# Performance work log

Measured on AMD Instinct MI355X. Metric: run time of the kernel, lower is better.

The kernel has to match this reference:

```python
import jax, jax.numpy as jnp
import numpy as np
from jax import lax


def _conv2d(x, w, b, pad):
    out = lax.conv_general_dilated(x, w, window_strides=(1, 1),
                                   padding=[(pad, pad), (pad, pad)])
    return out + b[None, :, None, None]


def _modulated_deform_conv(x, off_w, off_b, w, b, k, pad):
    """Modulated deformable conv (deformable_groups=1, stride=1, 'same' pad)."""
    B, C, H, W = x.shape
    K2 = k * k
    # offset/mask conv: 3*K2 channels -> (dy, dx, mask_logits)
    om = _conv2d(x, off_w, off_b, pad)              # [B, 3*K2, H, W]
    dy, dx, mlog = om[:, :K2], om[:, K2:2 * K2], om[:, 2 * K2:]
    mask = jax.nn.sigmoid(mlog)                     # [B, K2, H, W]

    xp = jnp.pad(x, ((0, 0), (0, 0), (pad, pad), (pad, pad)))
    Hp, Wp = H + 2 * pad, W + 2 * pad
    Ho, Wo = H, W                                   # stride 1, pad = k//2

    ky, kx = jnp.meshgrid(jnp.arange(k), jnp.arange(k), indexing='ij')
    ky = ky.reshape(1, K2, 1, 1).astype(x.dtype)
    kx = kx.reshape(1, K2, 1, 1).astype(x.dtype)
    iy = jnp.arange(Ho, dtype=x.dtype).reshape(1, 1, Ho, 1)
    ix = jnp.arange(Wo, dtype=x.dtype).reshape(1, 1, 1, Wo)

    py = iy + ky + dy                               # [B, K2, Ho, Wo] sample y (padded coords)
    px = ix + kx + dx                               # [B, K2, Ho, Wo] sample x

    y0f = jnp.floor(py); x0f = jnp.floor(px)
    ty = py - y0f; tx = px - x0f
    y0 = y0f.astype(jnp.int32); x0 = x0f.astype(jnp.int32)
    y1 = y0 + 1; x1 = x0 + 1

    xp_flat = xp.reshape(B, C, Hp * Wp)

    def gather(yi, xi):
        valid = ((yi >= 0) & (yi < Hp) & (xi >= 0) & (xi < Wp)).astype(x.dtype)
        yc = jnp.clip(yi, 0, Hp - 1)
        xc = jnp.clip(xi, 0, Wp - 1)
        idx = (yc * Wp + xc).reshape(B, 1, K2 * Ho * Wo)
        v = jnp.take_along_axis(xp_flat, idx, axis=2).reshape(B, C, K2, Ho, Wo)
        return v * valid[:, None]                   # zero-pad outside

    w00 = ((1 - ty) * (1 - tx))[:, None]
    w01 = ((1 - ty) * tx)[:, None]
    w10 = (ty * (1 - tx))[:, None]
    w11 = (ty * tx)[:, None]

    cols = (gather(y0, x0) * w00 + gather(y0, x1) * w01 +
            gather(y1, x0) * w10 + gather(y1, x1) * w11)
    cols = cols * mask[:, None]                     # [B, C, K2, Ho, Wo]

    O = w.shape[0]
    out = jnp.einsum('bckhw,ock->bohw', cols, w.reshape(O, C, K2))
    return out + b[None, :, None, None]


def setup_inputs() -> dict:
    key = jax.random.key(0)
    ks = jax.random.split(key, 12)
    B, Cin, H, W = 8, 64, 56, 56
    Ch = 128  # out_channels // 2

    def rn(k, shape, scale):
        return jax.random.normal(k, shape, dtype=jnp.float32) * scale

    return {
        'x': rn(ks[0], (B, Cin, H, W), 1.0),
        'w3': rn(ks[1], (Ch, Cin, 3, 3), 0.05),
        'b3': rn(ks[2], (Ch,), 0.05),
        'off3_w': rn(ks[3], (3 * 9, Cin, 3, 3), 0.01),
        'off3_b': rn(ks[4], (3 * 9,), 0.01),
        'w5': rn(ks[5], (Ch, Cin, 5, 5), 0.03),
        'b5': rn(ks[6], (Ch,), 0.05),
        'off5_w': rn(ks[7], (3 * 25, Cin, 5, 5), 0.01),
        'off5_b': rn(ks[8], (3 * 25,), 0.01),
        'sub_w': rn(ks[9], (Ch, Cin, 1, 1), 0.1),
        'sub_b': rn(ks[10], (Ch,), 0.05),
    }


def reference(x, w3, b3, off3_w, off3_b, w5, b5, off5_w, off5_b, sub_w, sub_b):
    x3 = _modulated_deform_conv(x, off3_w, off3_b, w3, b3, k=3, pad=1)
    x5 = _modulated_deform_conv(x, off5_w, off5_b, w5, b5, k=5, pad=2)
    xs = _conv2d(x, sub_w, sub_b, pad=0)            # 1x1 shortcut projection
    x3 = x3 + xs
    x5 = x5 + xs
    out = jnp.concatenate((x3, x5), axis=1)
    return jax.nn.relu(out)
```

## Files before the change

kernel.cpp:

```cpp
#include <hip/hip_runtime.h>
#include <hip/hip_bf16.h>
#include <math.h>

typedef __attribute__((ext_vector_type(8))) short short8;
typedef __attribute__((ext_vector_type(4))) float f32x4;

#define US_XP    0
#define N_XP     (8*60*60*64)
#define US_WOFF  (US_XP + N_XP)
#define N_WOFF   (26*2*8*64*8)
#define US_W5    (US_WOFF + N_WOFF)
#define N_W5     (26*2*8*64*8)
#define US_W3    (US_W5 + N_W5)
#define N_W3     (10*2*8*64*8)
#define US_TOT   (US_W3 + N_W3)
#define FB_BYTES (((US_TOT*2) + 15) & ~15)
#define F_BOM    0
#define F_B5     128
#define F_B3     256
#define N_ITEMS  (8*34*3136)
#define F_OFFS   384
#define F_WTS    (F_OFFS + N_ITEMS*4)

__device__ __forceinline__ unsigned short f2bf(float f) {
    union { float f; unsigned u; } v; v.f = f;
    unsigned r = v.u + 0x7FFFu + ((v.u >> 16) & 1u);
    return (unsigned short)(r >> 16);
}
__device__ __forceinline__ unsigned pack2(float lo, float hi) {
    __hip_bfloat162 h = __float22bfloat162_rn(make_float2(lo, hi));
    return *(unsigned*)&h;
}
__device__ __forceinline__ unsigned blend2(unsigned a, unsigned b, unsigned c, unsigned d,
                                           float w00, float w01, float w10, float w11) {
    float lo = __uint_as_float(a << 16) * w00 + __uint_as_float(b << 16) * w01
             + __uint_as_float(c << 16) * w10 + __uint_as_float(d << 16) * w11;
    float hi = __uint_as_float(a & 0xffff0000u) * w00 + __uint_as_float(b & 0xffff0000u) * w01
             + __uint_as_float(c & 0xffff0000u) * w10 + __uint_as_float(d & 0xffff0000u) * w11;
    return pack2(lo, hi);
}

__global__ __launch_bounds__(256) void xpose(const float* __restrict__ x,
                                             unsigned short* __restrict__ xp)
{
    __shared__ float ld[64*65];
    const int b   = blockIdx.y;
    const int px0 = blockIdx.x * 64;
    const int t   = threadIdx.x;
#pragma unroll
    for (int c0 = 0; c0 < 64; c0 += 4) {
        const int c = c0 + (t >> 6);
        const int p = t & 63;
        ld[c*65 + p] = x[((size_t)(b*64 + c))*3136 + px0 + p];
    }
    __syncthreads();
    const int lp = t >> 2;
    const int ch0 = (t & 3) * 16;
    const int px = px0 + lp;
    const int oy = px/56, ox = px - oy*56;
    unsigned short* dst = xp + ((size_t)b*3600 + (oy+2)*60 + (ox+2))*64 + ch0;
    unsigned short tmp[16];
#pragma unroll
    for (int k = 0; k < 16; ++k) tmp[k] = f2bf(ld[(ch0 + k)*65 + lp]);
    *(uint4*)dst       = *(uint4*)&tmp[0];
    *(uint4*)(dst + 8) = *(uint4*)&tmp[8];
}

__global__ __launch_bounds__(256) void prep_w(
    const float* __restrict__ w3, const float* __restrict__ b3,
    const float* __restrict__ off3w, const float* __restrict__ off3b,
    const float* __restrict__ w5, const float* __restrict__ b5,
    const float* __restrict__ off5w, const float* __restrict__ off5b,
    const float* __restrict__ subw, const float* __restrict__ subb,
    unsigned short* __restrict__ us, float* __restrict__ fb)
{
    const int NTOT = US_TOT + 384;
    for (int i = US_WOFF + blockIdx.x*256 + threadIdx.x; i < NTOT; i += gridDim.x*256) {
        if (i < US_TOT) {
            float v = 0.f;
            int j, mode;
            if (i < US_W5)      { j = i - US_WOFF; mode = 0; }
            else if (i < US_W3) { j = i - US_W5;   mode = 1; }
            else                { j = i - US_W3;   mode = 2; }
            int j8   = j & 7;
            int lane = (j >> 3) & 63;
            int oct  = (j >> 9) & 7;
            int kt   = (j >> 12) & 1;
            int tap  = j >> 13;
            int oc   = oct*16 + (lane & 15);
            int c    = kt*32 + (lane >> 4)*8 + j8;
            if (mode == 0) {
                if (oc < 27 && tap < 25) {
                    int ky = tap/5, kx = tap%5;
                    if (ky>=1 && ky<=3 && kx>=1 && kx<=3)
                        v = off3w[((oc*64 + c)*3 + (ky-1))*3 + (kx-1)];
                } else if (oc >= 27 && oc < 102 && tap < 25) {
                    v = off5w[((oc-27)*64 + c)*25 + tap];
                }
            } else if (mode == 1) {
                v = (tap < 25) ? w5[(oc*64 + c)*25 + tap] : subw[oc*64 + c];
            } else {
                v = (tap < 9) ? w3[(oc*64 + c)*9 + tap] : subw[oc*64 + c];
            }
            us[i] = f2bf(v);
        } else {
            int fj = i - US_TOT;
            float v;
            if (fj < 128)      v = (fj < 27) ? off3b[fj] : ((fj < 102) ? off5b[fj-27] : 0.f);
            else if (fj < 256) { int o = fj-128; v = b5[o] + subb[o]; }
            else               { int o = fj-256; v = b3[o] + subb[o]; }
            fb[fj] = v;
        }
    }
}

__global__ __launch_bounds__(256, 6) void convo3(
    const unsigned short* __restrict__ xp,
    const unsigned short* __restrict__ wp, const float* __restrict__ bias,
    int4* __restrict__ offs, uint2* __restrict__ wts)
{
    const int b    = blockIdx.y;
    const int pix0 = blockIdx.x * 32;
    const int lane = threadIdx.x & 63;
    const int wave = threadIdx.x >> 6;
    const int r15 = lane & 15, q4 = lane >> 4;
    const int cg  = lane & 7,  pr = lane >> 3;

    __shared__ __align__(16) unsigned short cols[2][2][32*72];

    f32x4 acc[2][2] = {{{0.f,0.f,0.f,0.f},{0.f,0.f,0.f,0.f}},
                       {{0.f,0.f,0.f,0.f},{0.f,0.f,0.f,0.f}}};

    const char* xb = (const char*)(xp + (size_t)b*(60*60*64));
    const int px  = wave*8 + pr;
    const int pix = pix0 + px;
    const int oy  = pix/56, ox = pix - oy*56;
    const int coff = (((oy+2)*60) + ox + 2) << 7;

    uint4 G0, G1;
    auto issue = [&](int ta, int tb) {
        int ka = 0, kb = 0;
        if (ta < 25) { int ky = ta/5, kx = ta - ky*5; ka = ((ky-2)*60 + (kx-2)) << 7; }
        if (tb < 25) { int ky = tb/5, kx = tb - ky*5; kb = ((ky-2)*60 + (kx-2)) << 7; }
        G0 = *(const uint4*)(xb + coff + ka + cg*16);
        G1 = *(const uint4*)(xb + coff + kb + cg*16);
    };
    auto commit = [&](unsigned short* bufa, unsigned short* bufb) {
        *(uint4*)&bufa[px*72 + cg*8] = G0;
        *(uint4*)&bufb[px*72 + cg*8] = G1;
    };
    auto gemm = [&](int tap, const unsigned short* buf) {
#pragma unroll
        for (int kt = 0; kt < 2; ++kt) {
            short8 A0 = *(const short8*)(wp + ((size_t)((tap*2+kt)*8 + wave*2    )*64 + lane)*8);
            short8 A1 = *(const short8*)(wp + ((size_t)((tap*2+kt)*8 + wave*2 + 1)*64 + lane)*8);
#pragma unroll
            for (int pt = 0; pt < 2; ++pt) {
                short8 Bf = *(const short8*)(buf + (pt*16 + r15)*72 + kt*32 + q4*8);
                acc[0][pt] = __builtin_amdgcn_mfma_f32_16x16x32_bf16(A0, Bf, acc[0][pt], 0, 0, 0);
                acc[1][pt] = __builtin_amdgcn_mfma_f32_16x16x32_bf16(A1, Bf, acc[1][pt], 0, 0, 0);
            }
        }
    };

    issue(0, 1);
    commit(cols[0][0], cols[0][1]);
    __syncthreads();
    for (int r = 0; r < 13; ++r) {
        if (r + 1 < 13) issue(2*r+2, 2*r+3);
        gemm(2*r,   cols[r&1][0]);
        gemm(2*r+1, cols[r&1][1]);
        if (r + 1 < 13) commit(cols[(r+1)&1][0], cols[(r+1)&1][1]);
        __syncthreads();
    }

    float* omt = (float*)cols;
#pragma unroll
    for (int i = 0; i < 2; ++i)
#pragma unroll
    for (int pt = 0; pt < 2; ++pt)
#pragma unroll
    for (int reg = 0; reg < 4; ++reg) {
        const int oc = (wave*2 + i)*16 + q4*4 + reg;
        const int p2 = pt*16 + r15;
        omt[oc*32 + p2] = acc[i][pt][reg] + bias[oc];
    }
    __syncthreads();

    const int tid = threadIdx.x;
#pragma unroll
    for (int itr = 0; itr < 5; ++itr) {
        const int idx = itr*256 + tid;
        if (idx >= 34*32) break;
        const int t  = idx >> 5;
        const int p2 = idx & 31;
        const int pix2 = pix0 + p2;
        const int oy2 = pix2/56, ox2 = pix2 - oy2*56;
        int ky, kx, cdy, cdx, cml, HP, SH;
        if (t < 25) { ky = t/5; kx = t%5; cdy = 27+t; cdx = 52+t; cml = 77+t; HP = 60; SH = 0; }
        else { int tt = t-25; ky = tt/3; kx = tt%3; cdy = tt; cdx = 9+tt; cml = 18+tt; HP = 58; SH = 1; }
        const float dy = omt[cdy*32 + p2];
        const float dx = omt[cdx*32 + p2];
        const float ml = omt[cml*32 + p2];
        const float mask = 1.f / (1.f + __expf(-ml));
        const float py = (float)(oy2 + ky) + dy;
        const float qx = (float)(ox2 + kx) + dx;
        const float y0f = floorf(py), x0f = floorf(qx);
        const float ty = py - y0f, tx = qx - x0f;
        const int y0 = (int)y0f, x0 = (int)x0f, y1 = y0+1, x1 = x0+1;
        float w00 = (1.f-ty)*(1.f-tx)*mask;
        float w01 = (1.f-ty)*tx*mask;
        float w10 = ty*(1.f-tx)*mask;
        float w11 = ty*tx*mask;
        const bool vy0 = (unsigned)y0 < (unsigned)HP, vy1 = (unsigned)y1 < (unsigned)HP;
        const bool vx0 = (unsigned)x0 < (unsigned)HP, vx1 = (unsigned)x1 < (unsigned)HP;
        if (!(vy0 && vx0)) w00 = 0.f;
        if (!(vy0 && vx1)) w01 = 0.f;
        if (!(vy1 && vx0)) w10 = 0.f;
        if (!(vy1 && vx1)) w11 = 0.f;
        const int yc0 = min(max(y0,0),HP-1)+SH, yc1 = min(max(y1,0),HP-1)+SH;
        const int xc0 = min(max(x0,0),HP-1)+SH, xc1 = min(max(x1,0),HP-1)+SH;
        const int mi = (b*34 + t)*3136 + pix2;
        offs[mi] = make_int4((yc0*60+xc0)<<7, (yc0*60+xc1)<<7, (yc1*60+xc0)<<7, (yc1*60+xc1)<<7);
        wts[mi]  = make_uint2(pack2(w00,w01), pack2(w10,w11));
    }
}

__global__ __launch_bounds__(256, 3) void convd5(
    const unsigned short* __restrict__ xp,
    const int4* __restrict__ offs, const uint2* __restrict__ wts,
    float* __restrict__ out,
    const unsigned short* __restrict__ wp5, const float* __restrict__ bias5,
    const unsigned short* __restrict__ wp3, const float* __restrict__ bias3)
{
    const int kind = blockIdx.z;
    const unsigned short* wp = kind ? wp3 : wp5;
    const float* bias = kind ? bias3 : bias5;
    const int R     = kind ? 5  : 13;
    const int K2    = kind ? 9  : 25;
    const int tofs  = kind ? 25 : 0;
    const int outc0 = kind ? 0  : 128;

    const int b    = blockIdx.y;
    const int pix0 = blockIdx.x * 32;
    const int lane = threadIdx.x & 63;
    const int wave = threadIdx.x >> 6;
    const int r15 = lane & 15, q4 = lane >> 4;
    const int cg  = lane & 7,  pr = lane >> 3;

    __shared__ __align__(16) unsigned short cols[2][2][32*72];

    f32x4 acc[2][2] = {{{0.f,0.f,0.f,0.f},{0.f,0.f,0.f,0.f}},
                       {{0.f,0.f,0.f,0.f},{0.f,0.f,0.f,0.f}}};

    const char* xb = (const char*)(xp + (size_t)b*(60*60*64));
    const int px  = wave*8 + pr;
    const int pix = pix0 + px;
    const int oy  = pix/56, ox = pix - oy*56;
    const int coff  = (((oy+2)*60) + ox + 2) << 7;
    const int mbase = (b*34 + tofs)*3136 + pix;

    uint4 C0[4], C1[4];
    uint2 WC0, WC1;
    int4  MOc0, MOc1, MOn0, MOn1;
    uint2 MWc0, MWc1, MWn0, MWn1;
    short8 Aa[8];

    auto loadMetaN = [&](int ta, int tb) {
        const int a  = min(ta, K2-1) * 3136;
        const int bb = min(tb, K2-1) * 3136;
        MOn0 = offs[mbase + a];  MWn0 = wts[mbase + a];
        MOn1 = offs[mbase + bb]; MWn1 = wts[mbase + bb];
    };
    auto issue = [&](int ta, int tb) {
        if (ta >= K2) {
            C0[0] = *(const uint4*)(xb + coff + cg*16);
        } else {
            WC0 = MWc0;
            C0[0] = *(const uint4*)(xb + MOc0.x + cg*16);
            C0[1] = *(const uint4*)(xb + MOc0.y + cg*16);
            C0[2] = *(const uint4*)(xb + MOc0.z + cg*16);
            C0[3] = *(const uint4*)(xb + MOc0.w + cg*16);
        }
        if (tb >= K2) {
            C1[0] = *(const uint4*)(xb + coff + cg*16);
        } else {
            WC1 = MWc1;
            C1[0] = *(const uint4*)(xb + MOc1.x + cg*16);
            C1[1] = *(const uint4*)(xb + MOc1.y + cg*16);
            C1[2] = *(const uint4*)(xb + MOc1.z + cg*16);
            C1[3] = *(const uint4*)(xb + MOc1.w + cg*16);
        }
    };
    auto commit = [&](int ta, int tb, unsigned short* ba, unsigned short* bb) {
        uint4 res;
        if (ta >= K2) {
            res = C0[0];
        } else {
            const float w00 = __uint_as_float(WC0.x << 16);
            const float w01 = __uint_as_float(WC0.x & 0xffff0000u);
            const float w10 = __uint_as_float(WC0.y << 16);
            const float w11 = __uint_as_float(WC0.y & 0xffff0000u);
            res.x = blend2(C0[0].x, C0[1].x, C0[2].x, C0[3].x, w00, w01, w10, w11);
            res.y = blend2(C0[0].y, C0[1].y, C0[2].y, C0[3].y, w00, w01, w10, w11);
            res.z = blend2(C0[0].z, C0[1].z, C0[2].z, C0[3].z, w00, w01, w10, w11);
            res.w = blend2(C0[0].w, C0[1].w, C0[2].w, C0[3].w, w00, w01, w10, w11);
        }
        *(uint4*)&ba[px*72 + cg*8] = res;
        if (tb >= K2) {
            res = C1[0];
        } else {
            const float w00 = __uint_as_float(WC1.x << 16);
            const float w01 = __uint_as_float(WC1.x & 0xffff0000u);
            const float w10 = __uint_as_float(WC1.y << 16);
            const float w11 = __uint_as_float(WC1.y & 0xffff0000u);
            res.x = blend2(C1[0].x, C1[1].x, C1[2].x, C1[3].x, w00, w01, w10, w11);
            res.y = blend2(C1[0].y, C1[1].y, C1[2].y, C1[3].y, w00, w01, w10, w11);
            res.z = blend2(C1[0].z, C1[1].z, C1[2].z, C1[3].z, w00, w01, w10, w11);
            res.w = blend2(C1[0].w, C1[1].w, C1[2].w, C1[3].w, w00, w01, w10, w11);
        }
        *(uint4*)&bb[px*72 + cg*8] = res;
    };
    auto loadA = [&](int r) {
#pragma unroll
        for (int tt = 0; tt < 2; ++tt)
#pragma unroll
        for (int kt = 0; kt < 2; ++kt)
#pragma unroll
        for (int i = 0; i < 2; ++i)
            Aa[tt*4+kt*2+i] = *(const short8*)(wp + ((size_t)(((2*r+tt)*2+kt)*8 + wave*2 + i)*64 + lane)*8);
    };
    auto gemmT = [&](int tt, const unsigned short* buf) {
#pragma unroll
        for (int kt = 0; kt < 2; ++kt)
#pragma unroll
            for (int pt = 0; pt < 2; ++pt) {
                short8 B = *(const short8*)(buf + (pt*16 + r15)*72 + kt*32 + q4*8);
                acc[0][pt] = __builtin_amdgcn_mfma_f32_16x16x32_bf16(Aa[tt*4+kt*2+0], B, acc[0][pt], 0, 0, 0);
                acc[1][pt] = __builtin_amdgcn_mfma_f32_16x16x32_bf16(Aa[tt*4+kt*2+1], B, acc[1][pt], 0, 0, 0);
            }
    };

    loadMetaN(0, 1);
    MOc0 = MOn0; MWc0 = MWn0; MOc1 = MOn1; MWc1 = MWn1;
    issue(0, 1);
    loadMetaN(2, 3);
    loadA(0);
    commit(0, 1, cols[0][0], cols[0][1]);
    __syncthreads();

    for (int r = 0; r < R; ++r) {
        const bool more = (r + 1 < R);
        if (more) {
            MOc0 = MOn0; MWc0 = MWn0; MOc1 = MOn1; MWc1 = MWn1;
            issue(2*r+2, 2*r+3);
            loadMetaN(2*r+4, 2*r+5);
        }
        gemmT(0, cols[r&1][0]);
        gemmT(1, cols[r&1][1]);
        if (more) {
            loadA(r + 1);
            commit(2*r+2, 2*r+3, cols[(r+1)&1][0], cols[(r+1)&1][1]);
        }
        __syncthreads();
    }

#pragma unroll
    for (int i = 0; i < 2; ++i)
#pragma unroll
    for (int pt = 0; pt < 2; ++pt)
#pragma unroll
    for (int reg = 0; reg < 4; ++reg) {
        const int oc = (wave*2 + i)*16 + q4*4 + reg;
        const int p2 = pix0 + pt*16 + r15;
        float v = fmaxf(acc[i][pt][reg] + bias[oc], 0.f);
        out[((size_t)b*256 + outc0 + oc)*3136 + p2] = v;
    }
}

extern "C" void kernel_launch(void* const* d_in, const int* in_sizes, int n_in,
                              void* d_out, int out_size, void* d_ws, size_t ws_size,
                              hipStream_t stream)
{
    (void)in_sizes; (void)n_in; (void)out_size; (void)ws_size;
    const float* x     = (const float*)d_in[0];
    const float* w3    = (const float*)d_in[1];
    const float* b3    = (const float*)d_in[2];
    const float* off3w = (const float*)d_in[3];
    const float* off3b = (const float*)d_in[4];
    const float* w5    = (const float*)d_in[5];
    const float* b5    = (const float*)d_in[6];
    const float* off5w = (const float*)d_in[7];
    const float* off5b = (const float*)d_in[8];
    const float* subw  = (const float*)d_in[9];
    const float* subb  = (const float*)d_in[10];

    unsigned short* us = (unsigned short*)d_ws;
    float* fb   = (float*)((char*)d_ws + FB_BYTES);
    int4*  offs = (int4*)(fb + F_OFFS);
    uint2* wts  = (uint2*)(fb + F_WTS);
    float* out  = (float*)d_out;

    hipMemsetAsync(us + US_XP, 0, (size_t)N_XP * 2, stream);
    xpose<<<dim3(49, 8), dim3(256), 0, stream>>>(x, us + US_XP);
    prep_w<<<dim3(512), dim3(256), 0, stream>>>(
        w3, b3, off3w, off3b, w5, b5, off5w, off5b, subw, subb, us, fb);

    convo3<<<dim3(98, 8), dim3(256), 0, stream>>>(
        us + US_XP, us + US_WOFF, fb + F_BOM, offs, wts);

    convd5<<<dim3(98, 8, 2), dim3(256), 0, stream>>>(
        us + US_XP, offs, wts, out,
        us + US_W5, fb + F_B5, us + US_W3, fb + F_B3);
}
```

Measured before the change: 156.8 us.

## Switch to fp16 storage with packed-half bilinear blend, fold border zeroing into xpose

Stores the activations, weights and bilinear weights as fp16 instead of bf16 and uses the f16 MFMA, so the bilinear blend can run on packed half2 math rather than unpacking to fp32 and repacking. The full-buffer memset is replaced by an extra xpose block per batch that zeroes only the 2-pixel padding border. The register-prefetched A operand in the deformable conv is dropped in favour of loading weights inside the gemm loop, which lowers register pressure but exposes load latency. fp16 has a narrower range than bf16 and the blend now accumulates in half precision, which reduces accuracy.

```diff
diff --git a/kernel.cpp b/kernel.cpp
--- a/kernel.cpp
+++ b/kernel.cpp
@@ -1,8 +1,8 @@
 #include <hip/hip_runtime.h>
-#include <hip/hip_bf16.h>
 #include <math.h>
 
-typedef __attribute__((ext_vector_type(8))) short short8;
+typedef _Float16 half8 __attribute__((ext_vector_type(8)));
+typedef _Float16 half2v __attribute__((ext_vector_type(2)));
 typedef __attribute__((ext_vector_type(4))) float f32x4;
 
 #define US_XP    0
@@ -22,29 +22,42 @@
 #define F_OFFS   384
 #define F_WTS    (F_OFFS + N_ITEMS*4)
 
-__device__ __forceinline__ unsigned short f2bf(float f) {
-    union { float f; unsigned u; } v; v.f = f;
-    unsigned r = v.u + 0x7FFFu + ((v.u >> 16) & 1u);
-    return (unsigned short)(r >> 16);
-}
-__device__ __forceinline__ unsigned pack2(float lo, float hi) {
-    __hip_bfloat162 h = __float22bfloat162_rn(make_float2(lo, hi));
-    return *(unsigned*)&h;
-}
-__device__ __forceinline__ unsigned blend2(unsigned a, unsigned b, unsigned c, unsigned d,
-                                           float w00, float w01, float w10, float w11) {
-    float lo = __uint_as_float(a << 16) * w00 + __uint_as_float(b << 16) * w01
-             + __uint_as_float(c << 16) * w10 + __uint_as_float(d << 16) * w11;
-    float hi = __uint_as_float(a & 0xffff0000u) * w00 + __uint_as_float(b & 0xffff0000u) * w01
-             + __uint_as_float(c & 0xffff0000u) * w10 + __uint_as_float(d & 0xffff0000u) * w11;
-    return pack2(lo, hi);
+__device__ __forceinline__ unsigned short f2h(float f) {
+    union { _Float16 h; unsigned short s; } c; c.h = (_Float16)f; return c.s;
+}
+__device__ __forceinline__ half2v splat_lo(unsigned u) {
+    union { unsigned short s; _Float16 h; } c; c.s = (unsigned short)(u & 0xffffu);
+    return (half2v){c.h, c.h};
+}
+__device__ __forceinline__ half2v splat_hi(unsigned u) {
+    union { unsigned short s; _Float16 h; } c; c.s = (unsigned short)(u >> 16);
+    return (half2v){c.h, c.h};
+}
+__device__ __forceinline__ unsigned blendh(unsigned a, unsigned b, unsigned c, unsigned d,
+                                           half2v W00, half2v W01, half2v W10, half2v W11) {
+    union { unsigned u; half2v h; } A, B, C, D, R;
+    A.u = a; B.u = b; C.u = c; D.u = d;
+    R.h = A.h*W00 + B.h*W01 + C.h*W10 + D.h*W11;
+    return R.u;
 }
 
 __global__ __launch_bounds__(256) void xpose(const float* __restrict__ x,
                                              unsigned short* __restrict__ xp)
 {
+    const int b = blockIdx.y;
+    if (blockIdx.x == 49) {
+        const uint4 z = make_uint4(0,0,0,0);
+        for (int i = threadIdx.x; i < 464*8; i += 256) {
+            const int px = i >> 3, part = i & 7;
+            int oy, ox;
+            if (px < 120)      { oy = px/60;            ox = px%60; }
+            else if (px < 240) { int j = px-120; oy = 58 + j/60; ox = j%60; }
+            else               { int j = px-240; oy = 2 + (j>>2); ox = ((j&2)?58:0) + (j&1); }
+            *(uint4*)(xp + ((size_t)b*3600 + oy*60 + ox)*64 + part*8) = z;
+        }
+        return;
+    }
     __shared__ float ld[64*65];
-    const int b   = blockIdx.y;
     const int px0 = blockIdx.x * 64;
     const int t   = threadIdx.x;
 #pragma unroll
@@ -61,7 +74,7 @@
     unsigned short* dst = xp + ((size_t)b*3600 + (oy+2)*60 + (ox+2))*64 + ch0;
     unsigned short tmp[16];
 #pragma unroll
-    for (int k = 0; k < 16; ++k) tmp[k] = f2bf(ld[(ch0 + k)*65 + lp]);
+    for (int k = 0; k < 16; ++k) tmp[k] = f2h(ld[(ch0 + k)*65 + lp]);
     *(uint4*)dst       = *(uint4*)&tmp[0];
     *(uint4*)(dst + 8) = *(uint4*)&tmp[8];
 }
@@ -102,7 +115,7 @@
             } else {
                 v = (tap < 9) ? w3[(oc*64 + c)*9 + tap] : subw[oc*64 + c];
             }
-            us[i] = f2bf(v);
+            us[i] = f2h(v);
         } else {
             int fj = i - US_TOT;
             float v;
@@ -114,7 +127,7 @@
     }
 }
 
-__global__ __launch_bounds__(256, 6) void convo3(
+__global__ __launch_bounds__(256, 6) void convo7(
     const unsigned short* __restrict__ xp,
     const unsigned short* __restrict__ wp, const float* __restrict__ bias,
     int4* __restrict__ offs, uint2* __restrict__ wts)
@@ -152,13 +165,13 @@
     auto gemm = [&](int tap, const unsigned short* buf) {
 #pragma unroll
         for (int kt = 0; kt < 2; ++kt) {
-            short8 A0 = *(const short8*)(wp + ((size_t)((tap*2+kt)*8 + wave*2    )*64 + lane)*8);
-            short8 A1 = *(const short8*)(wp + ((size_t)((tap*2+kt)*8 + wave*2 + 1)*64 + lane)*8);
+            half8 A0 = *(const half8*)(wp + ((size_t)((tap*2+kt)*8 + wave*2    )*64 + lane)*8);
+            half8 A1 = *(const half8*)(wp + ((size_t)((tap*2+kt)*8 + wave*2 + 1)*64 + lane)*8);
 #pragma unroll
             for (int pt = 0; pt < 2; ++pt) {
-                short8 Bf = *(const short8*)(buf + (pt*16 + r15)*72 + kt*32 + q4*8);
-                acc[0][pt] = __builtin_amdgcn_mfma_f32_16x16x32_bf16(A0, Bf, acc[0][pt], 0, 0, 0);
-                acc[1][pt] = __builtin_amdgcn_mfma_f32_16x16x32_bf16(A1, Bf, acc[1][pt], 0, 0, 0);
+                half8 Bf = *(const half8*)(buf + (pt*16 + r15)*72 + kt*32 + q4*8);
+                acc[0][pt] = __builtin_amdgcn_mfma_f32_16x16x32_f16(A0, Bf, acc[0][pt], 0, 0, 0);
+                acc[1][pt] = __builtin_amdgcn_mfma_f32_16x16x32_f16(A1, Bf, acc[1][pt], 0, 0, 0);
             }
         }
     };
@@ -222,11 +235,12 @@
         const int xc0 = min(max(x0,0),HP-1)+SH, xc1 = min(max(x1,0),HP-1)+SH;
         const int mi = (b*34 + t)*3136 + pix2;
         offs[mi] = make_int4((yc0*60+xc0)<<7, (yc0*60+xc1)<<7, (yc1*60+xc0)<<7, (yc1*60+xc1)<<7);
-        wts[mi]  = make_uint2(pack2(w00,w01), pack2(w10,w11));
-    }
-}
-
-__global__ __launch_bounds__(256, 3) void convd5(
+        wts[mi]  = make_uint2((unsigned)f2h(w00) | ((unsigned)f2h(w01) << 16),
+                              (unsigned)f2h(w10) | ((unsigned)f2h(w11) << 16));
+    }
+}
+
+__global__ __launch_bounds__(256, 3) void convd7(
     const unsigned short* __restrict__ xp,
     const int4* __restrict__ offs, const uint2* __restrict__ wts,
     float* __restrict__ out,
@@ -264,7 +278,6 @@
     uint2 WC0, WC1;
     int4  MOc0, MOc1, MOn0, MOn1;
     uint2 MWc0, MWc1, MWn0, MWn1;
-    short8 Aa[8];
 
     auto loadMetaN = [&](int ta, int tb) {
         const int a  = min(ta, K2-1) * 3136;
@@ -297,55 +310,44 @@
         if (ta >= K2) {
             res = C0[0];
         } else {
-            const float w00 = __uint_as_float(WC0.x << 16);
-            const float w01 = __uint_as_float(WC0.x & 0xffff0000u);
-            const float w10 = __uint_as_float(WC0.y << 16);
-            const float w11 = __uint_as_float(WC0.y & 0xffff0000u);
-            res.x = blend2(C0[0].x, C0[1].x, C0[2].x, C0[3].x, w00, w01, w10, w11);
-            res.y = blend2(C0[0].y, C0[1].y, C0[2].y, C0[3].y, w00, w01, w10, w11);
-            res.z = blend2(C0[0].z, C0[1].z, C0[2].z, C0[3].z, w00, w01, w10, w11);
-            res.w = blend2(C0[0].w, C0[1].w, C0[2].w, C0[3].w, w00, w01, w10, w11);
+            const half2v W00 = splat_lo(WC0.x), W01 = splat_hi(WC0.x);
+            const half2v W10 = splat_lo(WC0.y), W11 = splat_hi(WC0.y);
+            res.x = blendh(C0[0].x, C0[1].x, C0[2].x, C0[3].x, W00, W01, W10, W11);
+            res.y = blendh(C0[0].y, C0[1].y, C0[2].y, C0[3].y, W00, W01, W10, W11);
+            res.z = blendh(C0[0].z, C0[1].z, C0[2].z, C0[3].z, W00, W01, W10, W11);
+            res.w = blendh(C0[0].w, C0[1].w, C0[2].w, C0[3].w, W00, W01, W10, W11);
         }
         *(uint4*)&ba[px*72 + cg*8] = res;
         if (tb >= K2) {
             res = C1[0];
         } else {
-            const float w00 = __uint_as_float(WC1.x << 16);
-            const float w01 = __uint_as_float(WC1.x & 0xffff0000u);
-            const float w10 = __uint_as_float(WC1.y << 16);
-            const float w11 = __uint_as_float(WC1.y & 0xffff0000u);
-            res.x = blend2(C1[0].x, C1[1].x, C1[2].x, C1[3].x, w00, w01, w10, w11);
-            res.y = blend2(C1[0].y, C1[1].y, C1[2].y, C1[3].y, w00, w01, w10, w11);
-            res.z = blend2(C1[0].z, C1[1].z, C1[2].z, C1[3].z, w00, w01, w10, w11);
-            res.w = blend2(C1[0].w, C1[1].w, C1[2].w, C1[3].w, w00, w01, w10, w11);
+            const half2v W00 = splat_lo(WC1.x), W01 = splat_hi(WC1.x);
+            const half2v W10 = splat_lo(WC1.y), W11 = splat_hi(WC1.y);
+            res.x = blendh(C1[0].x, C1[1].x, C1[2].x, C1[3].x, W00, W01, W10, W11);
+            res.y = blendh(C1[0].y, C1[1].y, C1[2].y, C1[3].y, W00, W01, W10, W11);
+            res.z = blendh(C1[0].z, C1[1].z, C1[2].z, C1[3].z, W00, W01, W10, W11);
+            res.w = blendh(C1[0].w, C1[1].w, C1[2].w, C1[3].w, W00, W01, W10, W11);
         }
         *(uint4*)&bb[px*72 + cg*8] = res;
     };
-    auto loadA = [&](int r) {
-#pragma unroll
-        for (int tt = 0; tt < 2; ++tt)
-#pragma unroll
-        for (int kt = 0; kt < 2; ++kt)
-#pragma unroll
-        for (int i = 0; i < 2; ++i)
-            Aa[tt*4+kt*2+i] = *(const short8*)(wp + ((size_t)(((2*r+tt)*2+kt)*8 + wave*2 + i)*64 + lane)*8);
-    };
-    auto gemmT = [&](int tt, const unsigned short* buf) {
-#pragma unroll
-        for (int kt = 0; kt < 2; ++kt)
+    auto gemm = [&](int tap, const unsigned short* buf) {
+#pragma unroll
+        for (int kt = 0; kt < 2; ++kt) {
+            half8 A0 = *(const half8*)(wp + ((size_t)((tap*2+kt)*8 + wave*2    )*64 + lane)*8);
+            half8 A1 = *(const half8*)(wp + ((size_t)((tap*2+kt)*8 + wave*2 + 1)*64 + lane)*8);
 #pragma unroll
             for (int pt = 0; pt < 2; ++pt) {
-                short8 B = *(const short8*)(buf + (pt*16 + r15)*72 + kt*32 + q4*8);
-                acc[0][pt] = __builtin_amdgcn_mfma_f32_16x16x32_bf16(Aa[tt*4+kt*2+0], B, acc[0][pt], 0, 0, 0);
-                acc[1][pt] = __builtin_amdgcn_mfma_f32_16x16x32_bf16(Aa[tt*4+kt*2+1], B, acc[1][pt], 0, 0, 0);
+                half8 B = *(const half8*)(buf + (pt*16 + r15)*72 + kt*32 + q4*8);
+                acc[0][pt] = __builtin_amdgcn_mfma_f32_16x16x32_f16(A0, B, acc[0][pt], 0, 0, 0);
+                acc[1][pt] = __builtin_amdgcn_mfma_f32_16x16x32_f16(A1, B, acc[1][pt], 0, 0, 0);
             }
+        }
     };
 
     loadMetaN(0, 1);
     MOc0 = MOn0; MWc0 = MWn0; MOc1 = MOn1; MWc1 = MWn1;
     issue(0, 1);
     loadMetaN(2, 3);
-    loadA(0);
     commit(0, 1, cols[0][0], cols[0][1]);
     __syncthreads();
 
@@ -356,12 +358,9 @@
             issue(2*r+2, 2*r+3);
             loadMetaN(2*r+4, 2*r+5);
         }
-        gemmT(0, cols[r&1][0]);
-        gemmT(1, cols[r&1][1]);
-        if (more) {
-            loadA(r + 1);
-            commit(2*r+2, 2*r+3, cols[(r+1)&1][0], cols[(r+1)&1][1]);
-        }
+        gemm(2*r,   cols[r&1][0]);
+        gemm(2*r+1, cols[r&1][1]);
+        if (more) commit(2*r+2, 2*r+3, cols[(r+1)&1][0], cols[(r+1)&1][1]);
         __syncthreads();
     }
 
@@ -401,15 +400,14 @@
     uint2* wts  = (uint2*)(fb + F_WTS);
     float* out  = (float*)d_out;
 
-    hipMemsetAsync(us + US_XP, 0, (size_t)N_XP * 2, stream);
-    xpose<<<dim3(49, 8), dim3(256), 0, stream>>>(x, us + US_XP);
+    xpose<<<dim3(50, 8), dim3(256), 0, stream>>>(x, us + US_XP);
     prep_w<<<dim3(512), dim3(256), 0, stream>>>(
         w3, b3, off3w, off3b, w5, b5, off5w, off5b, subw, subb, us, fb);
 
-    convo3<<<dim3(98, 8), dim3(256), 0, stream>>>(
+    convo7<<<dim3(98, 8), dim3(256), 0, stream>>>(
         us + US_XP, us + US_WOFF, fb + F_BOM, offs, wts);
 
-    convd5<<<dim3(98, 8, 2), dim3(256), 0, stream>>>(
+    convd7<<<dim3(98, 8, 2), dim3(256), 0, stream>>>(
         us + US_XP, offs, wts, out,
         us + US_W5, fb + F_B5, us + US_W3, fb + F_B3);
 }
```

New measurement: 153.6 us. 2.1% less time.
